# Optimization experiments

Hardware: AMD Instinct MI355X
Metric: run time of the kernel (lower is better)

## Reference

```python
import jax, jax.numpy as jnp
import numpy as np

T_LEN, BATCH, IN_SIZE, HID = 512, 64, 1024, 1024
EPS = 1e-6


def layer_norm(x, alpha, beta, eps=EPS):
    # Matches torch: mean over last dim, UNBIASED variance (ddof=1)
    mu = jnp.mean(x, axis=-1, keepdims=True)
    var = jnp.var(x, axis=-1, keepdims=True, ddof=1)
    xn = (x - mu) / jnp.sqrt(var + eps)
    return alpha * xn + beta


def setup_inputs() -> dict:
    key = jax.random.key(0)
    ks = jax.random.split(key, 12)
    std = 1.0 / np.sqrt(HID)
    u = lambda k, shape: jax.random.uniform(k, shape, jnp.float32, -std, std)
    return {
        "x": jax.random.normal(ks[0], (T_LEN, BATCH, IN_SIZE), jnp.float32),
        "Wi": u(ks[1], (4 * HID, IN_SIZE)),
        "bi": u(ks[2], (4 * HID,)),
        "Wh": u(ks[3], (4 * HID, HID)),
        "bh": u(ks[4], (4 * HID,)),
        "g_i2h": u(ks[5], (4 * HID,)),
        "b_i2h": u(ks[6], (4 * HID,)),
        "g_h2h": u(ks[7], (4 * HID,)),
        "b_h2h": u(ks[8], (4 * HID,)),
        "g_cell": u(ks[9], (HID,)),
        "b_cell": u(ks[10], (HID,)),
    }


def reference(x, Wi, bi, Wh, bh, g_i2h, b_i2h, g_h2h, b_h2h, g_cell, b_cell):
    # Faithful to the source: h and c are NEVER updated inside the loop
    # (the original code omits h = h_t / c = c_t), so every timestep sees
    # the initial zero state -> fully parallel over time.
    T, B, _ = x.shape
    H = Wh.shape[1]
    h0 = jnp.zeros((B, H), x.dtype)
    c0 = jnp.zeros((B, H), x.dtype)

    i2h = layer_norm(jnp.einsum('tbi,gi->tbg', x, Wi) + bi, g_i2h, b_i2h)  # [T,B,4H]
    h2h = layer_norm(h0 @ Wh.T + bh, g_h2h, b_h2h)                          # [B,4H]
    preact = i2h + h2h                                                      # [T,B,4H]

    gates = jax.nn.sigmoid(preact[..., :3 * H])
    g_t = jnp.tanh(preact[..., 3 * H:])
    f_t = gates[..., H:2 * H]
    o_t = gates[..., 2 * H:3 * H]
    # i_t = gates[..., :H] is computed in the original but unused

    c_t = c0 * f_t + (1.0 - f_t) * g_t
    c_t = layer_norm(c_t, g_cell, b_cell)
    h_t = o_t * jnp.tanh(c_t)  # [T,B,H]

    return h_t, h_t[-1]
```

## Files before the change

### kernel.cpp

```cpp
#include <hip/hip_runtime.h>
#include <hip/hip_bf16.h>
#include <stdint.h>


#define MROWS 32768L
#define NCOLS 4096
#define KDIM  1024

typedef __bf16 bf16x8 __attribute__((ext_vector_type(8)));
typedef __bf16 bf16x4 __attribute__((ext_vector_type(4)));
typedef float  f32x4  __attribute__((ext_vector_type(4)));

__device__ float g_Cvec[4096];

__device__ __forceinline__ void gload16(char* lds, const char* g) {
  __builtin_amdgcn_global_load_lds(
      (const __attribute__((address_space(1))) char*)g,
      (__attribute__((address_space(3))) char*)lds, 16, 0, 0);
}

__device__ __forceinline__ void block_reduce2(float& a, float& b, float* red, int tid) {
#pragma unroll
  for (int m = 32; m > 0; m >>= 1) {
    a += __shfl_xor(a, m, 64);
    b += __shfl_xor(b, m, 64);
  }
  const int lane = tid & 63, wid = tid >> 6;
  if (lane == 0) { red[wid] = a; red[4 + wid] = b; }
  __syncthreads();
  a = red[0] + red[1] + red[2] + red[3];
  b = red[4] + red[5] + red[6] + red[7];
  __syncthreads();
}

__global__ __launch_bounds__(256) void cast_kernel(const float4* __restrict__ in,
                                                   bf16x4* __restrict__ out, int n4) {
  int i = blockIdx.x * 256 + threadIdx.x;
  const int stride = gridDim.x * 256;
  for (; i < n4; i += stride) {
    const float4 v = in[i];
    bf16x4 o = { (__bf16)v.x, (__bf16)v.y, (__bf16)v.z, (__bf16)v.w };
    out[i] = o;
  }
}

__global__ __launch_bounds__(256) void prep_kernel(const float* __restrict__ bh,
                                                   const float* __restrict__ b_i2h,
                                                   const float* __restrict__ g_h2h,
                                                   const float* __restrict__ b_h2h) {
  __shared__ float red[8];
  const int tid = threadIdx.x;
  float v[16];
  float s = 0.f, ss = 0.f;
#pragma unroll
  for (int u = 0; u < 16; ++u) {
    v[u] = bh[tid + u * 256];
    s += v[u]; ss += v[u] * v[u];
  }
  block_reduce2(s, ss, red, tid);
  const float mu  = s * (1.f / 4096.f);
  const float var = (ss - 4096.f * mu * mu) * (1.f / 4095.f);
  const float rs  = rsqrtf(var + 1e-6f);
#pragma unroll
  for (int u = 0; u < 16; ++u) {
    const int g = tid + u * 256;
    g_Cvec[g] = b_i2h[g] + g_h2h[g] * ((v[u] - mu) * rs) + b_h2h[g];
  }
}


#define LGKM0() do { asm volatile("s_waitcnt lgkmcnt(0)" ::: "memory"); \
    __builtin_amdgcn_sched_barrier(0); } while (0)
#define LGKM8() asm volatile("s_waitcnt lgkmcnt(8)" ::: "memory")
#define BAR()   __builtin_amdgcn_s_barrier()
#define VMCNT(n) asm volatile("s_waitcnt vmcnt(" #n ")" ::: "memory")
#define SETP1() __builtin_amdgcn_s_setprio(1)
#define SETP0() __builtin_amdgcn_s_setprio(0)

#define STG_A(s, h) { char* d_ = Al + (((s) & 1) << 15) + ((h) << 14); \
    const char* g_ = Ag + (long)(h) * 262144 + (s) * 128; \
    gload16(d_, g_); gload16(d_ + 8192, g_ + 131072); }

#define STG_B(s, h) { char* d_ = Bl + (((s) & 1) << 15) + ((h) << 14); \
    const char* g_ = Bg + (long)(h) * 262144 + (s) * 128; \
    gload16(d_, g_); gload16(d_ + 8192, g_ + 131072); }

#define ABASE(t) ((const char*)As + (((t) & 1) << 15) + (wr << 14))
#define BBASE(t) ((const char*)Bs + (((t) & 1) << 15) + ((wc >> 1) << 14))

#define RD_Ax(arr, Ahalf, c) { _Pragma("unroll") for (int mi_ = 0; mi_ < 4; ++mi_) { \
    const char* p_ = (Ahalf) + (((c) * 64 + mi_ * 16 + fr) << 7); \
    arr[mi_][0] = *(const bf16x8*)(p_ + cb0); \
    arr[mi_][1] = *(const bf16x8*)(p_ + cb1); } }

#define RD_Bx(arr, Bhalf, g) { _Pragma("unroll") for (int nj_ = 0; nj_ < 2; ++nj_) { \
    const char* p_ = (Bhalf) + ((brow0 + (g) * 32 + nj_ * 16 + fr) << 7); \
    arr[nj_][0] = *(const bf16x8*)(p_ + cb0); \
    arr[nj_][1] = *(const bf16x8*)(p_ + cb1); } }

#define MMQ(X, Y, c, g) { _Pragma("unroll") for (int mi_ = 0; mi_ < 4; ++mi_) { \
    _Pragma("unroll") for (int nj_ = 0; nj_ < 2; ++nj_) { \
      acc[(c)*4+mi_][(g)*2+nj_] = __builtin_amdgcn_mfma_f32_16x16x32_bf16( \
          X[mi_][0], Y[nj_][0], acc[(c)*4+mi_][(g)*2+nj_], 0, 0, 0); \
      acc[(c)*4+mi_][(g)*2+nj_] = __builtin_amdgcn_mfma_f32_16x16x32_bf16( \
          X[mi_][1], Y[nj_][1], acc[(c)*4+mi_][(g)*2+nj_], 0, 0, 0); } } }

#define TWOTILE(t, S0, S1, S2, VMA, VMB) { \
    const char* At_ = ABASE(t); const char* Bt_ = BBASE(t); \
    const char* Au_ = ABASE((t) + 1); const char* Bu_ = BBASE((t) + 1); \
     RD_Ax(A0, At_, 0); RD_Bx(B01, Bt_, 0); if (S0) STG_B((t) + 1, 1); \
           LGKM8(); BAR(); LGKM0(); SETP1(); MMQ(A0, B01, 0, 0); SETP0(); BAR(); \
     RD_Ax(A1, At_, 1); if (S1) STG_A((t) + 2, 0); \
           BAR(); LGKM0(); SETP1(); MMQ(A1, B01, 1, 0); SETP0(); BAR(); \
     RD_Bx(B23, Bt_, 1); if (S1) STG_A((t) + 2, 1); \
           BAR(); LGKM0(); SETP1(); MMQ(A1, B23, 1, 1); SETP0(); BAR(); \
     if (S1) STG_B((t) + 2, 0); VMA; \
           BAR(); LGKM0(); SETP1(); MMQ(A0, B23, 0, 1); SETP0(); BAR(); \
     RD_Ax(A0, Au_, 0); RD_Bx(B01, Bu_, 0); if (S1) STG_B((t) + 2, 1); \
           LGKM8(); BAR(); LGKM0(); SETP1(); MMQ(A0, B01, 0, 0); SETP0(); BAR(); \
     RD_Ax(A1, Au_, 1); if (S2) STG_A((t) + 3, 0); \
           BAR(); LGKM0(); SETP1(); MMQ(A1, B01, 1, 0); SETP0(); BAR(); \
     RD_Bx(B23, Bu_, 1); if (S2) STG_A((t) + 3, 1); \
           BAR(); LGKM0(); SETP1(); MMQ(A1, B23, 1, 1); SETP0(); BAR(); \
     if (S2) STG_B((t) + 3, 0); VMB; \
           BAR(); LGKM0(); SETP1(); MMQ(A0, B23, 0, 1); SETP0(); BAR(); }

__global__ __launch_bounds__(512, 2) void gemm_kernel(const __bf16* __restrict__ A,
                                                      const __bf16* __restrict__ B,
                                                      __bf16* __restrict__ Y, long r0) {
  __shared__ __align__(16) __bf16 As[2 * 2 * 8192];
  __shared__ __align__(16) __bf16 Bs[2 * 2 * 8192];

  const int tid  = threadIdx.x;
  const int lane = tid & 63;
  const int wid  = tid >> 6;
  const int wr   = wid >> 2;
  const int wc   = wid & 3;

  const int nwg = gridDim.x;
  const int q8 = nwg >> 3, r8 = nwg & 7;
  const int xcd = blockIdx.x & 7, rest = blockIdx.x >> 3;
  const int wgid = (xcd < r8 ? xcd * (q8 + 1) : r8 * (q8 + 1) + (xcd - r8) * q8) + rest;
  const long m0 = (long)(wgid >> 4) * 256;
  const long n0 = (long)(wgid & 15) * 256;

  const int scol = (((tid & 7) ^ ((tid >> 3) & 7)) << 4);
  const char* Ag = (const char*)(A + (r0 + m0) * KDIM) + (long)(tid >> 3) * 2048 + scol;
  const char* Bg = (const char*)(B + n0 * KDIM) + (long)(tid >> 3) * 2048 + scol;
  char* Al = (char*)As + tid * 16;
  char* Bl = (char*)Bs + tid * 16;

  const int fr  = lane & 15;
  const int sw  = (fr & 7) << 4;
  const int cb0 = (((lane >> 4) << 4)) ^ sw;
  const int cb1 = (64 | ((lane >> 4) << 4)) ^ sw;
  const int brow0 = (wc & 1) << 6;

  f32x4 acc[8][4];
  const f32x4 z = {0.f, 0.f, 0.f, 0.f};
#pragma unroll
  for (int i = 0; i < 8; ++i)
#pragma unroll
    for (int j = 0; j < 4; ++j) acc[i][j] = z;

  bf16x8 A0[4][2], A1[4][2], B01[2][2], B23[2][2];

  STG_A(0, 0); STG_A(0, 1); STG_B(0, 0); STG_B(0, 1);
  STG_A(1, 0); STG_A(1, 1); STG_B(1, 0);
  VMCNT(6);
  BAR();

#pragma unroll 1
  for (int tt = 0; tt < 7; ++tt) {
    const int t = tt * 2;
    TWOTILE(t, true, true, true, VMCNT(6), VMCNT(6));
  }
  TWOTILE(14, true, false, false, VMCNT(0), ((void)0));

  const long mrow = m0 + wr * 128 + ((lane >> 4) << 2);
  const long ncol = n0 + wc * 64 + fr;
  __bf16* Yp = Y + mrow * NCOLS + ncol;
#pragma unroll
  for (int c = 0; c < 2; ++c)
#pragma unroll
    for (int mi = 0; mi < 4; ++mi)
#pragma unroll
      for (int nj = 0; nj < 4; ++nj)
#pragma unroll
        for (int r = 0; r < 4; ++r)
          Yp[(long)(c * 64 + mi * 16 + r) * NCOLS + nj * 16] = (__bf16)acc[c * 4 + mi][nj][r];
}

__global__ __launch_bounds__(256) void pass2_kernel(const __bf16* __restrict__ Yw,
                                                    const float* __restrict__ bi,
                                                    const float* __restrict__ g_i2h,
                                                    const float* __restrict__ g_cell,
                                                    const float* __restrict__ b_cell,
                                                    float* __restrict__ out, long r0) {
  __shared__ float p0[4096];
  __shared__ float red[8];
  const int tid  = threadIdx.x;
  const long row = r0 + blockIdx.x;
  const bf16x8* yv = (const bf16x8*)(Yw + (long)blockIdx.x * NCOLS);

  float s = 0.f, ss = 0.f;
#pragma unroll
  for (int it = 0; it < 2; ++it) {
    const int ch = tid + it * 256;
    const bf16x8 v = yv[ch];
    const float4 b0 = ((const float4*)bi)[ch * 2];
    const float4 b1 = ((const float4*)bi)[ch * 2 + 1];
    float p[8];
    p[0] = (float)v[0] + b0.x;  p[1] = (float)v[1] + b0.y;
    p[2] = (float)v[2] + b0.z;  p[3] = (float)v[3] + b0.w;
    p[4] = (float)v[4] + b1.x;  p[5] = (float)v[5] + b1.y;
    p[6] = (float)v[6] + b1.z;  p[7] = (float)v[7] + b1.w;
#pragma unroll
    for (int u = 0; u < 8; ++u) {
      p0[ch * 8 + u] = p[u];
      s += p[u];
      ss += p[u] * p[u];
    }
  }
  block_reduce2(s, ss, red, tid);
  const float mu  = s * (1.f / 4096.f);
  const float var = (ss - 4096.f * mu * mu) * (1.f / 4095.f);
  const float rs  = rsqrtf(var + 1e-6f);

  float cc[4], oo[4];
  float s2 = 0.f, ss2 = 0.f;
#pragma unroll
  for (int u = 0; u < 4; ++u) {
    const int j = tid + u * 256;
    const float pf = g_i2h[1024 + j] * ((p0[1024 + j] - mu) * rs) + g_Cvec[1024 + j];
    const float po = g_i2h[2048 + j] * ((p0[2048 + j] - mu) * rs) + g_Cvec[2048 + j];
    const float pg = g_i2h[3072 + j] * ((p0[3072 + j] - mu) * rs) + g_Cvec[3072 + j];
    const float f  = 1.f / (1.f + __expf(-pf));
    oo[u] = 1.f / (1.f + __expf(-po));
    const float e2 = __expf(2.f * pg);
    const float gt = (e2 - 1.f) / (e2 + 1.f);
    cc[u] = (1.f - f) * gt;
    s2 += cc[u]; ss2 += cc[u] * cc[u];
  }
  block_reduce2(s2, ss2, red, tid);
  const float mu2  = s2 * (1.f / 1024.f);
  const float var2 = (ss2 - 1024.f * mu2 * mu2) * (1.f / 1023.f);
  const float rs2  = rsqrtf(var2 + 1e-6f);

  const long obase = row * 1024;
#pragma unroll
  for (int u = 0; u < 4; ++u) {
    const int j = tid + u * 256;
    const float cn = g_cell[j] * ((cc[u] - mu2) * rs2) + b_cell[j];
    const float e2 = __expf(2.f * cn);
    const float th = (e2 - 1.f) / (e2 + 1.f);
    const float h  = oo[u] * th;
    out[obase + j] = h;
    if (row >= MROWS - 64)
      out[MROWS * 1024 + ((row - (MROWS - 64)) << 10) + j] = h;
  }
}

extern "C" void kernel_launch(void* const* d_in, const int* in_sizes, int n_in,
                              void* d_out, int out_size, void* d_ws, size_t ws_size,
                              hipStream_t stream) {
  (void)in_sizes; (void)n_in; (void)out_size;
  const float* x      = (const float*)d_in[0];
  const float* Wi     = (const float*)d_in[1];
  const float* bi     = (const float*)d_in[2];
  const float* bh     = (const float*)d_in[4];
  const float* g_i2h  = (const float*)d_in[5];
  const float* b_i2h  = (const float*)d_in[6];
  const float* g_h2h  = (const float*)d_in[7];
  const float* b_h2h  = (const float*)d_in[8];
  const float* g_cell = (const float*)d_in[9];
  const float* b_cell = (const float*)d_in[10];
  float* out = (float*)d_out;

  __bf16* xb = (__bf16*)d_ws;
  __bf16* wb = (__bf16*)((char*)d_ws + 67108864);
  __bf16* y  = (__bf16*)((char*)d_ws + 75497472);

  cast_kernel<<<2048, 256, 0, stream>>>((const float4*)x, (bf16x4*)xb, 33554432 / 4);
  cast_kernel<<<1024, 256, 0, stream>>>((const float4*)Wi, (bf16x4*)wb, 4194304 / 4);
  prep_kernel<<<1, 256, 0, stream>>>(bh, b_i2h, g_h2h, b_h2h);

  long avail = (long)ws_size - 75497472L;
  long max_rows = (avail / (NCOLS * 2)) & ~255L;
  if (max_rows > 8192) max_rows = 8192;
  if (max_rows < 256)  max_rows = 256;
  for (long rbase = 0; rbase < MROWS; rbase += max_rows) {
    const long rows = (MROWS - rbase < max_rows) ? (MROWS - rbase) : max_rows;
    gemm_kernel<<<dim3((rows / 256) * 16), 512, 0, stream>>>(xb, wb, y, rbase);
    pass2_kernel<<<dim3(rows), 256, 0, stream>>>(y, bi, g_i2h, g_cell, b_cell, out, rbase);
  }
}
```

Before: 438.2 us.

## Switch GEMM inner loop to 32x32x16 MFMA tiles with reworked staging

Replaces the 16x16x32 bf16 MFMA fragments with 32x32x16 MFMA, changing the LDS read pattern, accumulator layout (f32x16) and epilogue store mapping. The global-to-LDS staging schedule is also regrouped so that both halves of A and of B are prefetched together, and the prologue and vmcnt thresholds are adjusted to match. The larger MFMA shape is meant to cut instruction count and LDS traffic per FLOP. The risks are different register pressure and the loss of the finer-grained interleaving between loads and compute.

Result: slower. 456.1 us (+4.1%).

```diff
diff --git a/kernel.cpp b/kernel.cpp
--- a/kernel.cpp
+++ b/kernel.cpp
@@ -10,6 +10,7 @@
 typedef __bf16 bf16x8 __attribute__((ext_vector_type(8)));
 typedef __bf16 bf16x4 __attribute__((ext_vector_type(4)));
 typedef float  f32x4  __attribute__((ext_vector_type(4)));
+typedef float  f32x16 __attribute__((ext_vector_type(16)));
 
 __device__ float g_Cvec[4096];
 
@@ -88,42 +89,40 @@
 #define ABASE(t) ((const char*)As + (((t) & 1) << 15) + (wr << 14))
 #define BBASE(t) ((const char*)Bs + (((t) & 1) << 15) + ((wc >> 1) << 14))
 
-#define RD_Ax(arr, Ahalf, c) { _Pragma("unroll") for (int mi_ = 0; mi_ < 4; ++mi_) { \
-    const char* p_ = (Ahalf) + (((c) * 64 + mi_ * 16 + fr) << 7); \
-    arr[mi_][0] = *(const bf16x8*)(p_ + cb0); \
-    arr[mi_][1] = *(const bf16x8*)(p_ + cb1); } }
-
-#define RD_Bx(arr, Bhalf, g) { _Pragma("unroll") for (int nj_ = 0; nj_ < 2; ++nj_) { \
-    const char* p_ = (Bhalf) + ((brow0 + (g) * 32 + nj_ * 16 + fr) << 7); \
-    arr[nj_][0] = *(const bf16x8*)(p_ + cb0); \
-    arr[nj_][1] = *(const bf16x8*)(p_ + cb1); } }
-
-#define MMQ(X, Y, c, g) { _Pragma("unroll") for (int mi_ = 0; mi_ < 4; ++mi_) { \
-    _Pragma("unroll") for (int nj_ = 0; nj_ < 2; ++nj_) { \
-      acc[(c)*4+mi_][(g)*2+nj_] = __builtin_amdgcn_mfma_f32_16x16x32_bf16( \
-          X[mi_][0], Y[nj_][0], acc[(c)*4+mi_][(g)*2+nj_], 0, 0, 0); \
-      acc[(c)*4+mi_][(g)*2+nj_] = __builtin_amdgcn_mfma_f32_16x16x32_bf16( \
-          X[mi_][1], Y[nj_][1], acc[(c)*4+mi_][(g)*2+nj_], 0, 0, 0); } } }
-
-#define TWOTILE(t, S0, S1, S2, VMA, VMB) { \
+#define RD_A32(arr, Ahalf, c) { _Pragma("unroll") for (int mi_ = 0; mi_ < 2; ++mi_) { \
+    const char* p_ = (Ahalf) + ((((c) * 2 + mi_) * 32 + r5) << 7); \
+    _Pragma("unroll") for (int ks_ = 0; ks_ < 4; ++ks_) \
+      arr[mi_][ks_] = *(const bf16x8*)(p_ + cbK[ks_]); } }
+
+#define RD_B32(arr, Bhalf, g) { \
+    const char* p_ = (Bhalf) + ((brow0 + (g) * 32 + r5) << 7); \
+    _Pragma("unroll") for (int ks_ = 0; ks_ < 4; ++ks_) \
+      arr[ks_] = *(const bf16x8*)(p_ + cbK[ks_]); }
+
+#define MMQ32(Aarr, Barr, c, g) { _Pragma("unroll") for (int mi_ = 0; mi_ < 2; ++mi_) { \
+    _Pragma("unroll") for (int ks_ = 0; ks_ < 4; ++ks_) \
+      acc[(c) * 2 + mi_][(g)] = __builtin_amdgcn_mfma_f32_32x32x16_bf16( \
+          Aarr[mi_][ks_], Barr[ks_], acc[(c) * 2 + mi_][(g)], 0, 0, 0); } }
+
+#define TWOTILE(t, S1, S2, VMA, VMB) { \
     const char* At_ = ABASE(t); const char* Bt_ = BBASE(t); \
     const char* Au_ = ABASE((t) + 1); const char* Bu_ = BBASE((t) + 1); \
-     RD_Ax(A0, At_, 0); RD_Bx(B01, Bt_, 0); if (S0) STG_B((t) + 1, 1); \
-           LGKM8(); BAR(); LGKM0(); SETP1(); MMQ(A0, B01, 0, 0); SETP0(); BAR(); \
-     RD_Ax(A1, At_, 1); if (S1) STG_A((t) + 2, 0); \
-           BAR(); LGKM0(); SETP1(); MMQ(A1, B01, 1, 0); SETP0(); BAR(); \
-     RD_Bx(B23, Bt_, 1); if (S1) STG_A((t) + 2, 1); \
-           BAR(); LGKM0(); SETP1(); MMQ(A1, B23, 1, 1); SETP0(); BAR(); \
-     if (S1) STG_B((t) + 2, 0); VMA; \
-           BAR(); LGKM0(); SETP1(); MMQ(A0, B23, 0, 1); SETP0(); BAR(); \
-     RD_Ax(A0, Au_, 0); RD_Bx(B01, Bu_, 0); if (S1) STG_B((t) + 2, 1); \
-           LGKM8(); BAR(); LGKM0(); SETP1(); MMQ(A0, B01, 0, 0); SETP0(); BAR(); \
-     RD_Ax(A1, Au_, 1); if (S2) STG_A((t) + 3, 0); \
-           BAR(); LGKM0(); SETP1(); MMQ(A1, B01, 1, 0); SETP0(); BAR(); \
-     RD_Bx(B23, Bu_, 1); if (S2) STG_A((t) + 3, 1); \
-           BAR(); LGKM0(); SETP1(); MMQ(A1, B23, 1, 1); SETP0(); BAR(); \
-     if (S2) STG_B((t) + 3, 0); VMB; \
-           BAR(); LGKM0(); SETP1(); MMQ(A0, B23, 0, 1); SETP0(); BAR(); }
+     RD_A32(Af0, At_, 0); RD_B32(Bf0, Bt_, 0); \
+           LGKM8(); BAR(); LGKM0(); SETP1(); MMQ32(Af0, Bf0, 0, 0); SETP0(); BAR(); \
+     RD_A32(Af1, At_, 1); \
+           BAR(); LGKM0(); SETP1(); MMQ32(Af1, Bf0, 1, 0); SETP0(); BAR(); \
+     RD_B32(Bf1, Bt_, 1); if (S1) { STG_A((t) + 2, 0); STG_A((t) + 2, 1); } \
+           BAR(); LGKM0(); SETP1(); MMQ32(Af1, Bf1, 1, 1); SETP0(); BAR(); \
+     if (S1) { STG_B((t) + 2, 0); STG_B((t) + 2, 1); } VMA; \
+           BAR(); LGKM0(); SETP1(); MMQ32(Af0, Bf1, 0, 1); SETP0(); BAR(); \
+     RD_A32(Af0, Au_, 0); RD_B32(Bf0, Bu_, 0); \
+           LGKM8(); BAR(); LGKM0(); SETP1(); MMQ32(Af0, Bf0, 0, 0); SETP0(); BAR(); \
+     RD_A32(Af1, Au_, 1); \
+           BAR(); LGKM0(); SETP1(); MMQ32(Af1, Bf0, 1, 0); SETP0(); BAR(); \
+     RD_B32(Bf1, Bu_, 1); if (S2) { STG_A((t) + 3, 0); STG_A((t) + 3, 1); } \
+           BAR(); LGKM0(); SETP1(); MMQ32(Af1, Bf1, 1, 1); SETP0(); BAR(); \
+     if (S2) { STG_B((t) + 3, 0); STG_B((t) + 3, 1); } VMB; \
+           BAR(); LGKM0(); SETP1(); MMQ32(Af0, Bf1, 0, 1); SETP0(); BAR(); }
 
 __global__ __launch_bounds__(512, 2) void gemm_kernel(const __bf16* __restrict__ A,
                                                       const __bf16* __restrict__ B,
@@ -150,45 +149,49 @@
   char* Al = (char*)As + tid * 16;
   char* Bl = (char*)Bs + tid * 16;
 
-  const int fr  = lane & 15;
-  const int sw  = (fr & 7) << 4;
-  const int cb0 = (((lane >> 4) << 4)) ^ sw;
-  const int cb1 = (64 | ((lane >> 4) << 4)) ^ sw;
+  const int r5  = lane & 31;
+  const int hi16 = (lane >> 5) << 4;
+  const int sw  = (lane & 7) << 4;
+  int cbK[4];
+#pragma unroll
+  for (int ks_ = 0; ks_ < 4; ++ks_) cbK[ks_] = (ks_ * 32 + hi16) ^ sw;
   const int brow0 = (wc & 1) << 6;
 
-  f32x4 acc[8][4];
-  const f32x4 z = {0.f, 0.f, 0.f, 0.f};
-#pragma unroll
-  for (int i = 0; i < 8; ++i)
-#pragma unroll
-    for (int j = 0; j < 4; ++j) acc[i][j] = z;
-
-  bf16x8 A0[4][2], A1[4][2], B01[2][2], B23[2][2];
+  f32x16 acc[4][2];
+#pragma unroll
+  for (int i = 0; i < 4; ++i)
+#pragma unroll
+    for (int j = 0; j < 2; ++j)
+#pragma unroll
+      for (int r = 0; r < 16; ++r) acc[i][j][r] = 0.f;
+
+  bf16x8 Af0[2][4], Af1[2][4], Bf0[4], Bf1[4];
 
   STG_A(0, 0); STG_A(0, 1); STG_B(0, 0); STG_B(0, 1);
-  STG_A(1, 0); STG_A(1, 1); STG_B(1, 0);
-  VMCNT(6);
+  STG_A(1, 0); STG_A(1, 1); STG_B(1, 0); STG_B(1, 1);
+  VMCNT(8);
   BAR();
 
 #pragma unroll 1
   for (int tt = 0; tt < 7; ++tt) {
     const int t = tt * 2;
-    TWOTILE(t, true, true, true, VMCNT(6), VMCNT(6));
-  }
-  TWOTILE(14, true, false, false, VMCNT(0), ((void)0));
-
-  const long mrow = m0 + wr * 128 + ((lane >> 4) << 2);
-  const long ncol = n0 + wc * 64 + fr;
-  __bf16* Yp = Y + mrow * NCOLS + ncol;
-#pragma unroll
-  for (int c = 0; c < 2; ++c)
-#pragma unroll
-    for (int mi = 0; mi < 4; ++mi)
-#pragma unroll
-      for (int nj = 0; nj < 4; ++nj)
-#pragma unroll
-        for (int r = 0; r < 4; ++r)
-          Yp[(long)(c * 64 + mi * 16 + r) * NCOLS + nj * 16] = (__bf16)acc[c * 4 + mi][nj][r];
+    TWOTILE(t, true, true, VMCNT(8), VMCNT(8));
+  }
+  TWOTILE(14, false, false, VMCNT(0), ((void)0));
+
+  const long mrowb = m0 + wr * 128;
+  const long ncolb = n0 + wc * 64 + r5;
+  const int  rhi   = (lane >> 5) << 2;
+  __bf16* Yp = Y + mrowb * NCOLS + ncolb;
+#pragma unroll
+  for (int i = 0; i < 4; ++i)
+#pragma unroll
+    for (int j = 0; j < 2; ++j)
+#pragma unroll
+      for (int r = 0; r < 16; ++r) {
+        const int rr = i * 32 + (r & 3) + ((r >> 2) << 3) + rhi;
+        Yp[(long)rr * NCOLS + j * 32] = (__bf16)acc[i][j][r];
+      }
 }
 
 __global__ __launch_bounds__(256) void pass2_kernel(const __bf16* __restrict__ Yw,
```
